# Performance work log

Hardware: AMD Instinct MI355X
Metric: run time of the kernel (lower is better)

## Reference

```python
import jax, jax.numpy as jnp
import numpy as np

S = 4          # num_residual_streams
B = 4          # batch
T = 4096       # seq_len
D = 1024       # dim
SINKHORN_ITERS = 20
EPS = 1e-05


def setup_inputs() -> dict:
    key = jax.random.key(0)
    k1, k2 = jax.random.split(key)
    residuals = jax.random.normal(k1, (B * S, T, D), dtype=jnp.float32)
    rmsnorm_weight = jnp.ones((D,), dtype=jnp.float32)
    # H_pre: -8 everywhere except layer_index % S = 0 -> 0.0
    H_pre_logits = jnp.full((S,), -8.0, dtype=jnp.float32).at[0].set(0.0)
    H_post_logits = jnp.zeros((S,), dtype=jnp.float32)
    # H_res: -8 off-diagonal, 0 on diagonal, plus alpha_init * noise
    H_res = (jnp.full((S, S), -8.0, dtype=jnp.float32) + 8.0 * jnp.eye(S, dtype=jnp.float32)
             + 0.01 * jax.random.normal(k2, (S, S), dtype=jnp.float32))
    return dict(residuals=residuals, rmsnorm_weight=rmsnorm_weight,
                H_pre_logits=H_pre_logits, H_post_logits=H_post_logits, H_res=H_res)


def _sinkhorn_knopp(M, num_iters, eps):
    # alternating row / column normalization to a doubly-stochastic matrix
    for _ in range(num_iters):
        M = M / (M.sum(axis=1, keepdims=True) + eps)
        M = M / (M.sum(axis=0, keepdims=True) + eps)
    return M


def reference(residuals, rmsnorm_weight, H_pre_logits, H_post_logits, H_res):
    s = H_pre_logits.shape[0]
    bs, t, d = residuals.shape
    b = bs // s
    # rearrange '(b s) t d -> (b t) s d'
    x = residuals.reshape(b, s, t, d).transpose(0, 2, 1, 3).reshape(b * t, s, d)
    # stream_aggregate with h_pre = sigmoid(H_pre_logits)
    h_pre = jax.nn.sigmoid(H_pre_logits)
    x_agg = jnp.einsum('nsd,s->nd', x, h_pre)
    # rmsnorm
    rms = jnp.sqrt(jnp.mean(x_agg * x_agg, axis=-1, keepdims=True) + EPS)
    x_norm = (x_agg / rms) * rmsnorm_weight
    # identity branch on the aggregated single-stream view
    branch_out = x_norm  # [(b t), d]
    # stream_distribute with h_post = 2 * sigmoid(H_post_logits)
    h_post = 2.0 * jax.nn.sigmoid(H_post_logits)
    y_dist = branch_out[:, None, :] * h_post[None, :, None]  # [(b t), s, d]
    # stream_mix with sinkhorn-normalized exp(H_res)
    M = _sinkhorn_knopp(jnp.exp(H_res), SINKHORN_ITERS, EPS)
    mixed = jnp.einsum('sr,nrd->nsd', M, y_dist)
    out = x + mixed
    # rearrange '(b t) s d -> (b s) t d'
    out = out.reshape(b, t, s, d).transpose(0, 2, 1, 3).reshape(b * s, t, d)
    return out
```

## Files before the change

### kernel.cpp

```cpp
#include <hip/hip_runtime.h>


#define S_ 4
#define T_ 4096
#define D_ 1024
#define NITER_ 20
#define EPSF_ 1e-5f

typedef float f32x4 __attribute__((ext_vector_type(4)));

__device__ float g_coef[8];

__global__ void hyperconn_coeff(const float* __restrict__ hpre_l,
                                const float* __restrict__ hpost_l,
                                const float* __restrict__ hres)
{
    if (threadIdx.x != 0) return;

    float M[S_][S_];
    #pragma unroll
    for (int i = 0; i < S_; ++i)
        #pragma unroll
        for (int j = 0; j < S_; ++j)
            M[i][j] = __expf(hres[i * S_ + j]);

    for (int it = 0; it < NITER_; ++it) {
        #pragma unroll
        for (int i = 0; i < S_; ++i) {
            float inv = 1.0f / (M[i][0] + M[i][1] + M[i][2] + M[i][3] + EPSF_);
            M[i][0] *= inv; M[i][1] *= inv; M[i][2] *= inv; M[i][3] *= inv;
        }
        #pragma unroll
        for (int j = 0; j < S_; ++j) {
            float inv = 1.0f / (M[0][j] + M[1][j] + M[2][j] + M[3][j] + EPSF_);
            M[0][j] *= inv; M[1][j] *= inv; M[2][j] *= inv; M[3][j] *= inv;
        }
    }

    #pragma unroll
    for (int s = 0; s < S_; ++s) {
        g_coef[s] = 1.0f / (1.0f + __expf(-hpre_l[s]));
        float c = 0.0f;
        #pragma unroll
        for (int r = 0; r < S_; ++r)
            c += M[s][r] * (2.0f / (1.0f + __expf(-hpost_l[r])));
        g_coef[S_ + s] = c;
    }
}

__global__ __launch_bounds__(256, 4) void hyperconn_main(
    const float* __restrict__ res,
    const float* __restrict__ w,
    float* __restrict__ out,
    const int n_rows)
{
    const int lane = threadIdx.x & 63;
    const int gw   = (int)((blockIdx.x * blockDim.x + threadIdx.x) >> 6);
    const int nw   = (int)((gridDim.x * blockDim.x) >> 6);

    const float h0 = g_coef[0], h1 = g_coef[1], h2 = g_coef[2], h3 = g_coef[3];
    const float cs0 = g_coef[4], cs1 = g_coef[5], cs2 = g_coef[6], cs3 = g_coef[7];
    const float cs[S_] = {cs0, cs1, cs2, cs3};

    const f32x4* res4 = reinterpret_cast<const f32x4*>(res);
    const f32x4* w4   = reinterpret_cast<const f32x4*>(w);
    f32x4*       out4 = reinterpret_cast<f32x4*>(out);

    const size_t sstride = (size_t)T_ * (D_ / 4);

    f32x4 wt[4];
    #pragma unroll
    for (int k = 0; k < 4; ++k)
        wt[k] = w4[(k << 6) + lane];

    for (int n = gw; n < n_rows; n += nw) {
        const int b = n >> 12;
        const int t = n & (T_ - 1);
        const size_t rb = ((size_t)(b * S_) * T_ + t) * (D_ / 4) + lane;

        f32x4 r[S_][4];
        #pragma unroll
        for (int s = 0; s < S_; ++s)
            #pragma unroll
            for (int k = 0; k < 4; ++k)
                r[s][k] = res4[rb + (size_t)s * sstride + (k << 6)];

        f32x4 agg[4];
        #pragma unroll
        for (int k = 0; k < 4; ++k)
            agg[k] = h0 * r[0][k] + h1 * r[1][k] + h2 * r[2][k] + h3 * r[3][k];

        float ssq = 0.0f;
        #pragma unroll
        for (int k = 0; k < 4; ++k)
            ssq += agg[k].x*agg[k].x + agg[k].y*agg[k].y
                 + agg[k].z*agg[k].z + agg[k].w*agg[k].w;
        #pragma unroll
        for (int off = 1; off <= 32; off <<= 1)
            ssq += __shfl_xor(ssq, off, 64);

        const float inv_rms = rsqrtf(ssq * (1.0f / (float)D_) + EPSF_);

        #pragma unroll
        for (int k = 0; k < 4; ++k) {
            const f32x4 nrm = agg[k] * inv_rms * wt[k];
            #pragma unroll
            for (int s = 0; s < S_; ++s)
                out4[rb + (size_t)s * sstride + (k << 6)] = r[s][k] + nrm * cs[s];
        }
    }
}

extern "C" void kernel_launch(void* const* d_in, const int* in_sizes, int n_in,
                              void* d_out, int out_size, void* d_ws, size_t ws_size,
                              hipStream_t stream) {
    const float* res     = (const float*)d_in[0];
    const float* weight  = (const float*)d_in[1];
    const float* hpre_l  = (const float*)d_in[2];
    const float* hpost_l = (const float*)d_in[3];
    const float* hres    = (const float*)d_in[4];
    float*       out     = (float*)d_out;

    hyperconn_coeff<<<1, 64, 0, stream>>>(hpre_l, hpost_l, hres);

    const int n_rows = in_sizes[0] / (S_ * D_);
    hyperconn_main<<<1024, 256, 0, stream>>>(res, weight, out, n_rows);
}
```

Baseline: 454.4 us.

## Assign one stream per wave and reduce streams through shared memory

Each 256-thread block now handles four consecutive tokens, and each wave owns one residual stream. Every wave reads a 16KB contiguous chunk of that stream instead of gathering four strided rows per token. The per-token stream aggregation runs as a rotating accumulate in LDS with barriers, and the RMS scale is shared through LDS. The grid grows from a fixed 1024 persistent blocks to one block per four tokens. The aim is more contiguous DRAM access and fewer grid-stride loop iterations, at the cost of extra LDS traffic and several __syncthreads per block.

```diff
diff --git a/kernel.cpp b/kernel.cpp
--- a/kernel.cpp
+++ b/kernel.cpp
@@ -51,62 +51,80 @@
 __global__ __launch_bounds__(256, 4) void hyperconn_main(
     const float* __restrict__ res,
     const float* __restrict__ w,
-    float* __restrict__ out,
-    const int n_rows)
+    float* __restrict__ out)
 {
     const int lane = threadIdx.x & 63;
-    const int gw   = (int)((blockIdx.x * blockDim.x + threadIdx.x) >> 6);
-    const int nw   = (int)((gridDim.x * blockDim.x) >> 6);
+    const int wv   = threadIdx.x >> 6;
+    const int n    = blockIdx.x;
+    const int b    = n >> 10;
+    const int t0   = (n & 1023) << 2;
 
-    const float h0 = g_coef[0], h1 = g_coef[1], h2 = g_coef[2], h3 = g_coef[3];
-    const float cs0 = g_coef[4], cs1 = g_coef[5], cs2 = g_coef[6], cs3 = g_coef[7];
-    const float cs[S_] = {cs0, cs1, cs2, cs3};
+    __shared__ __align__(16) float s_agg[4][D_];
+    __shared__ float s_inv[4];
+
+    const float h = g_coef[wv];
+    const float c = g_coef[4 + wv];
 
     const f32x4* res4 = reinterpret_cast<const f32x4*>(res);
     const f32x4* w4   = reinterpret_cast<const f32x4*>(w);
     f32x4*       out4 = reinterpret_cast<f32x4*>(out);
 
-    const size_t sstride = (size_t)T_ * (D_ / 4);
+    const int    D4   = D_ / 4;
+    const size_t base = ((size_t)(b * S_ + wv) * T_ + t0) * D4;
 
     f32x4 wt[4];
     #pragma unroll
     for (int k = 0; k < 4; ++k)
         wt[k] = w4[(k << 6) + lane];
 
-    for (int n = gw; n < n_rows; n += nw) {
-        const int b = n >> 12;
-        const int t = n & (T_ - 1);
-        const size_t rb = ((size_t)(b * S_) * T_ + t) * (D_ / 4) + lane;
-
-        f32x4 r[S_][4];
-        #pragma unroll
-        for (int s = 0; s < S_; ++s)
-            #pragma unroll
-            for (int k = 0; k < 4; ++k)
-                r[s][k] = res4[rb + (size_t)s * sstride + (k << 6)];
-
-        f32x4 agg[4];
+    f32x4 r[4][4];
+    #pragma unroll
+    for (int j = 0; j < 4; ++j)
         #pragma unroll
         for (int k = 0; k < 4; ++k)
-            agg[k] = h0 * r[0][k] + h1 * r[1][k] + h2 * r[2][k] + h3 * r[3][k];
+            r[j][k] = res4[base + j * D4 + (k << 6) + lane];
 
+    {
+        f32x4* dst = reinterpret_cast<f32x4*>(&s_agg[wv][0]);
+        #pragma unroll
+        for (int k = 0; k < 4; ++k)
+            dst[(k << 6) + lane] = h * r[wv][k];
+    }
+    __syncthreads();
+    #pragma unroll
+    for (int st = 1; st < 4; ++st) {
+        const int j = (wv + st) & 3;
+        f32x4* dst = reinterpret_cast<f32x4*>(&s_agg[j][0]);
+        #pragma unroll
+        for (int k = 0; k < 4; ++k)
+            dst[(k << 6) + lane] += h * r[j][k];
+        __syncthreads();
+    }
+
+    {
+        const f32x4* src = reinterpret_cast<const f32x4*>(&s_agg[wv][0]);
         float ssq = 0.0f;
         #pragma unroll
-        for (int k = 0; k < 4; ++k)
-            ssq += agg[k].x*agg[k].x + agg[k].y*agg[k].y
-                 + agg[k].z*agg[k].z + agg[k].w*agg[k].w;
+        for (int k = 0; k < 4; ++k) {
+            const f32x4 a = src[(k << 6) + lane];
+            ssq += a.x*a.x + a.y*a.y + a.z*a.z + a.w*a.w;
+        }
         #pragma unroll
         for (int off = 1; off <= 32; off <<= 1)
             ssq += __shfl_xor(ssq, off, 64);
+        if (lane == 0)
+            s_inv[wv] = rsqrtf(ssq * (1.0f / (float)D_) + EPSF_);
+    }
+    __syncthreads();
 
-        const float inv_rms = rsqrtf(ssq * (1.0f / (float)D_) + EPSF_);
-
+    #pragma unroll
+    for (int j = 0; j < 4; ++j) {
+        const float inv = s_inv[j];
+        const f32x4* aj = reinterpret_cast<const f32x4*>(&s_agg[j][0]);
         #pragma unroll
         for (int k = 0; k < 4; ++k) {
-            const f32x4 nrm = agg[k] * inv_rms * wt[k];
-            #pragma unroll
-            for (int s = 0; s < S_; ++s)
-                out4[rb + (size_t)s * sstride + (k << 6)] = r[s][k] + nrm * cs[s];
+            const f32x4 nrm = aj[(k << 6) + lane] * inv * wt[k];
+            out4[base + j * D4 + (k << 6) + lane] = r[j][k] + nrm * c;
         }
     }
 }
@@ -124,5 +142,5 @@
     hyperconn_coeff<<<1, 64, 0, stream>>>(hpre_l, hpost_l, hres);
 
     const int n_rows = in_sizes[0] / (S_ * D_);
-    hyperconn_main<<<1024, 256, 0, stream>>>(res, weight, out, n_rows);
+    hyperconn_main<<<n_rows >> 2, 256, 0, stream>>>(res, weight, out);
 }
```

Result: slower. 512.0 us (+12.7%).
